# Kernel optimization log

Hardware: AMD Instinct MI355X
Metric: run time of the kernel (lower is better)

Reference implementation:

```python
import jax, jax.numpy as jnp
import numpy as np
import math

N_BINS = 2  # K: exact-enumeration branch requires K**R <= 1024


def setup_inputs() -> dict:
    key = jax.random.key(0)
    # activity in [0,1): B=131072 samples, R=10 binary components -> K**R = 1024 joint states
    activity = jax.random.uniform(key, (131072, 10), dtype=jnp.float32)
    return {"activity": activity}


def reference(activity):
    B, R = activity.shape
    K = N_BINS
    # soft assignment for n_bins == 2: [B, R, K]
    soft_assign = jnp.stack([1.0 - activity, activity], axis=-1)
    # exact joint distribution via sequential outer-product expansion: [B, K**R]
    joint_p = soft_assign[:, 0, :]
    for r in range(1, R):  # fixed small structural loop over R components
        joint_p = (joint_p[:, :, None] * soft_assign[:, r, None, :]).reshape(B, -1)
    p_a = joint_p.mean(axis=0)                      # [K**R]
    p_a_safe = jnp.clip(p_a, 1e-12)
    log_k_p = jnp.log(p_a_safe) / math.log(K)       # log base K
    joint_h = -jnp.sum(p_a * log_k_p)
    return -joint_h
```

## Files before the change

### kernel.cpp

```cpp
#include <hip/hip_runtime.h>
#include <hip/hip_bf16.h>
#include <math.h>

#define NBINS   1024
#define NPART   1024
#define NCHUNK  32
#define LSTRIDE 72

typedef __attribute__((ext_vector_type(8)))  short short8;
typedef __attribute__((ext_vector_type(16))) float f32x16;


__global__ __launch_bounds__(128, 2) void hist_kernel(const float* __restrict__ act,
                                                      float* __restrict__ gC,
                                                      int rows)
{
    __shared__ ushort Phi_u[2][32][LSTRIDE];
    __shared__ ushort Plo_u[2][32][LSTRIDE];
    __shared__ float  C_lds[NBINS];

    const int tid  = threadIdx.x;
    const int wav  = tid >> 6;
    const int lane = tid & 63;

    const int row = blockIdx.x * 128 + tid;

    float v[10];
    float valid = 1.0f;
    if (row < rows) {
        const float2* a2 = (const float2*)(act + (size_t)row * 10);
        #pragma unroll
        for (int k = 0; k < 5; ++k) {
            float2 t = a2[k];
            v[2 * k] = t.x; v[2 * k + 1] = t.y;
        }
    } else {
        valid = 0.0f;
        #pragma unroll
        for (int k = 0; k < 10; ++k) v[k] = 0.0f;
    }

    float hi[32], lo[32];
    {
        float t2[2], t4[4], t8[8], t16[16];
        t2[0] = valid * (1.0f - v[0]); t2[1] = valid * v[0];
        #pragma unroll
        for (int k = 0; k < 4; ++k)  t4[k]  = t2[k >> 1]  * ((k & 1) ? v[1] : 1.0f - v[1]);
        #pragma unroll
        for (int k = 0; k < 8; ++k)  t8[k]  = t4[k >> 1]  * ((k & 1) ? v[2] : 1.0f - v[2]);
        #pragma unroll
        for (int k = 0; k < 16; ++k) t16[k] = t8[k >> 1]  * ((k & 1) ? v[3] : 1.0f - v[3]);
        #pragma unroll
        for (int k = 0; k < 32; ++k) hi[k]  = t16[k >> 1] * ((k & 1) ? v[4] : 1.0f - v[4]);
    }
    {
        float t2[2], t4[4], t8[8], t16[16];
        t2[0] = 1.0f - v[5]; t2[1] = v[5];
        #pragma unroll
        for (int k = 0; k < 4; ++k)  t4[k]  = t2[k >> 1]  * ((k & 1) ? v[6] : 1.0f - v[6]);
        #pragma unroll
        for (int k = 0; k < 8; ++k)  t8[k]  = t4[k >> 1]  * ((k & 1) ? v[7] : 1.0f - v[7]);
        #pragma unroll
        for (int k = 0; k < 16; ++k) t16[k] = t8[k >> 1]  * ((k & 1) ? v[8] : 1.0f - v[8]);
        #pragma unroll
        for (int k = 0; k < 32; ++k) lo[k]  = t16[k >> 1] * ((k & 1) ? v[9] : 1.0f - v[9]);
    }

    #pragma unroll
    for (int m = 0; m < 32; ++m) {
        __hip_bfloat16 bh = __float2bfloat16(hi[m]);
        __hip_bfloat16 bl = __float2bfloat16(lo[m]);
        Phi_u[wav][m][lane] = *(const ushort*)&bh;
        Plo_u[wav][m][lane] = *(const ushort*)&bl;
    }

    __syncthreads();

    const int m  = lane & 31;
    const int kh = (lane >> 5) * 8;

    f32x16 acc = {};
    #pragma unroll
    for (int t = 0; t < 4; ++t) {
        const short8 a = *(const short8*)&Phi_u[wav][m][kh + 16 * t];
        const short8 b = *(const short8*)&Plo_u[wav][m][kh + 16 * t];
        acc = __builtin_amdgcn_mfma_f32_32x32x16_bf16(a, b, acc, 0, 0, 0);
    }

    if (wav == 1) {
        #pragma unroll
        for (int r = 0; r < 16; ++r)
            C_lds[r * 64 + lane] = acc[r];
    }
    __syncthreads();
    if (wav == 0) {
        #pragma unroll
        for (int r = 0; r < 16; ++r)
            C_lds[r * 64 + lane] += acc[r];
    }
    __syncthreads();

    float4* dst4 = (float4*)(gC + (size_t)blockIdx.x * NBINS);
    const float4* src4 = (const float4*)C_lds;
    dst4[tid]       = src4[tid];
    dst4[tid + 128] = src4[tid + 128];
}

__global__ __launch_bounds__(256) void reduce_kernel(const float* __restrict__ gC,
                                                     float* __restrict__ g2)
{
    const int chunk = blockIdx.x >> 2;
    const int bin   = (blockIdx.x & 3) * 256 + threadIdx.x;
    const float* p  = gC + (size_t)chunk * 32 * NBINS + bin;
    float s = 0.0f;
    #pragma unroll
    for (int k = 0; k < 32; ++k) s += p[k * NBINS];
    g2[chunk * NBINS + bin] = s;
}

__global__ __launch_bounds__(256) void finalize_kernel(const float* __restrict__ g2,
                                                       float* __restrict__ out,
                                                       float invB)
{
    __shared__ float red[4];
    const int tid = threadIdx.x;

    float4 acc = make_float4(0.f, 0.f, 0.f, 0.f);
    #pragma unroll
    for (int s = 0; s < NCHUNK; ++s) {
        const float4 t = *(const float4*)&g2[s * NBINS + tid * 4];
        acc.x += t.x; acc.y += t.y; acc.z += t.z; acc.w += t.w;
    }

    float s = 0.0f;
    const float b[4] = {acc.x, acc.y, acc.z, acc.w};
    #pragma unroll
    for (int k = 0; k < 4; ++k) {
        const float p  = b[k] * invB;
        const float ps = fmaxf(p, 1e-12f);
        s += p * log2f(ps);
    }
    #pragma unroll
    for (int off = 32; off > 0; off >>= 1) s += __shfl_down(s, off);
    if ((tid & 63) == 0) red[tid >> 6] = s;
    __syncthreads();
    if (tid == 0) out[0] = red[0] + red[1] + red[2] + red[3];
}

extern "C" void kernel_launch(void* const* d_in, const int* in_sizes, int n_in,
                              void* d_out, int out_size, void* d_ws, size_t ws_size,
                              hipStream_t stream)
{
    const float* act = (const float*)d_in[0];
    const int rows = in_sizes[0] / 10;
    float* gC = (float*)d_ws;
    float* g2 = gC + 1024 * NBINS;

    hist_kernel<<<NPART, 128, 0, stream>>>(act, gC, rows);
    reduce_kernel<<<128, 256, 0, stream>>>(gC, g2);
    finalize_kernel<<<1, 256, 0, stream>>>(g2, (float*)d_out, 1.0f / (float)rows);
}
```

Baseline: 16.46 us.

## Process two row tiles per block to halve partial histograms

Each hist block now handles 256 rows in two sequential MFMA passes that share one accumulator, and the grid shrinks from 1024 to 512 blocks. This halves the partial-histogram traffic written to workspace and read back by the reduce kernel, which now sums 16 partials per chunk instead of 32. The cost is an extra pair of barriers and LDS reuse per block, less parallelism in the histogram stage, and higher register pressure from keeping both rows' inputs live.

```diff
diff --git a/kernel.cpp b/kernel.cpp
--- a/kernel.cpp
+++ b/kernel.cpp
@@ -3,44 +3,18 @@
 #include <math.h>
 
 #define NBINS   1024
-#define NPART   1024
+#define NPART   512
 #define NCHUNK  32
+#define PPC     16
 #define LSTRIDE 72
 
 typedef __attribute__((ext_vector_type(8)))  short short8;
 typedef __attribute__((ext_vector_type(16))) float f32x16;
 
 
-__global__ __launch_bounds__(128, 2) void hist_kernel(const float* __restrict__ act,
-                                                      float* __restrict__ gC,
-                                                      int rows)
+__device__ __forceinline__ void make_trees(const float v[10], float valid,
+                                           float hi[32], float lo[32])
 {
-    __shared__ ushort Phi_u[2][32][LSTRIDE];
-    __shared__ ushort Plo_u[2][32][LSTRIDE];
-    __shared__ float  C_lds[NBINS];
-
-    const int tid  = threadIdx.x;
-    const int wav  = tid >> 6;
-    const int lane = tid & 63;
-
-    const int row = blockIdx.x * 128 + tid;
-
-    float v[10];
-    float valid = 1.0f;
-    if (row < rows) {
-        const float2* a2 = (const float2*)(act + (size_t)row * 10);
-        #pragma unroll
-        for (int k = 0; k < 5; ++k) {
-            float2 t = a2[k];
-            v[2 * k] = t.x; v[2 * k + 1] = t.y;
-        }
-    } else {
-        valid = 0.0f;
-        #pragma unroll
-        for (int k = 0; k < 10; ++k) v[k] = 0.0f;
-    }
-
-    float hi[32], lo[32];
     {
         float t2[2], t4[4], t8[8], t16[16];
         t2[0] = valid * (1.0f - v[0]); t2[1] = valid * v[0];
@@ -65,26 +39,84 @@
         #pragma unroll
         for (int k = 0; k < 32; ++k) lo[k]  = t16[k >> 1] * ((k & 1) ? v[9] : 1.0f - v[9]);
     }
+}
 
-    #pragma unroll
-    for (int m = 0; m < 32; ++m) {
-        __hip_bfloat16 bh = __float2bfloat16(hi[m]);
-        __hip_bfloat16 bl = __float2bfloat16(lo[m]);
-        Phi_u[wav][m][lane] = *(const ushort*)&bh;
-        Plo_u[wav][m][lane] = *(const ushort*)&bl;
+__global__ __launch_bounds__(128, 2) void hist_kernel(const float* __restrict__ act,
+                                                      float* __restrict__ gC,
+                                                      int rows)
+{
+    __shared__ ushort Phi_u[2][32][LSTRIDE];
+    __shared__ ushort Plo_u[2][32][LSTRIDE];
+    __shared__ float  C_lds[NBINS];
+
+    const int tid  = threadIdx.x;
+    const int wav  = tid >> 6;
+    const int lane = tid & 63;
+
+    const int r0 = blockIdx.x * 256 + tid;
+    const int r1 = r0 + 128;
+
+    float v0[10], v1[10];
+    float valid0 = 1.0f, valid1 = 1.0f;
+    if (r0 < rows) {
+        const float2* a2 = (const float2*)(act + (size_t)r0 * 10);
+        #pragma unroll
+        for (int k = 0; k < 5; ++k) { float2 t = a2[k]; v0[2*k] = t.x; v0[2*k+1] = t.y; }
+    } else {
+        valid0 = 0.0f;
+        #pragma unroll
+        for (int k = 0; k < 10; ++k) v0[k] = 0.0f;
     }
-
-    __syncthreads();
+    if (r1 < rows) {
+        const float2* a2 = (const float2*)(act + (size_t)r1 * 10);
+        #pragma unroll
+        for (int k = 0; k < 5; ++k) { float2 t = a2[k]; v1[2*k] = t.x; v1[2*k+1] = t.y; }
+    } else {
+        valid1 = 0.0f;
+        #pragma unroll
+        for (int k = 0; k < 10; ++k) v1[k] = 0.0f;
+    }
 
     const int m  = lane & 31;
     const int kh = (lane >> 5) * 8;
+    f32x16 acc = {};
 
-    f32x16 acc = {};
-    #pragma unroll
-    for (int t = 0; t < 4; ++t) {
-        const short8 a = *(const short8*)&Phi_u[wav][m][kh + 16 * t];
-        const short8 b = *(const short8*)&Plo_u[wav][m][kh + 16 * t];
-        acc = __builtin_amdgcn_mfma_f32_32x32x16_bf16(a, b, acc, 0, 0, 0);
+    {
+        float hi[32], lo[32];
+        make_trees(v0, valid0, hi, lo);
+        #pragma unroll
+        for (int q = 0; q < 32; ++q) {
+            __hip_bfloat16 bh = __float2bfloat16(hi[q]);
+            __hip_bfloat16 bl = __float2bfloat16(lo[q]);
+            Phi_u[wav][q][lane] = *(const ushort*)&bh;
+            Plo_u[wav][q][lane] = *(const ushort*)&bl;
+        }
+        __syncthreads();
+        #pragma unroll
+        for (int t = 0; t < 4; ++t) {
+            const short8 a = *(const short8*)&Phi_u[wav][m][kh + 16 * t];
+            const short8 b = *(const short8*)&Plo_u[wav][m][kh + 16 * t];
+            acc = __builtin_amdgcn_mfma_f32_32x32x16_bf16(a, b, acc, 0, 0, 0);
+        }
+        __syncthreads();
+    }
+    {
+        float hi[32], lo[32];
+        make_trees(v1, valid1, hi, lo);
+        #pragma unroll
+        for (int q = 0; q < 32; ++q) {
+            __hip_bfloat16 bh = __float2bfloat16(hi[q]);
+            __hip_bfloat16 bl = __float2bfloat16(lo[q]);
+            Phi_u[wav][q][lane] = *(const ushort*)&bh;
+            Plo_u[wav][q][lane] = *(const ushort*)&bl;
+        }
+        __syncthreads();
+        #pragma unroll
+        for (int t = 0; t < 4; ++t) {
+            const short8 a = *(const short8*)&Phi_u[wav][m][kh + 16 * t];
+            const short8 b = *(const short8*)&Plo_u[wav][m][kh + 16 * t];
+            acc = __builtin_amdgcn_mfma_f32_32x32x16_bf16(a, b, acc, 0, 0, 0);
+        }
     }
 
     if (wav == 1) {
@@ -111,10 +143,10 @@
 {
     const int chunk = blockIdx.x >> 2;
     const int bin   = (blockIdx.x & 3) * 256 + threadIdx.x;
-    const float* p  = gC + (size_t)chunk * 32 * NBINS + bin;
+    const float* p  = gC + (size_t)chunk * PPC * NBINS + bin;
     float s = 0.0f;
     #pragma unroll
-    for (int k = 0; k < 32; ++k) s += p[k * NBINS];
+    for (int k = 0; k < PPC; ++k) s += p[k * NBINS];
     g2[chunk * NBINS + bin] = s;
 }
 
@@ -154,7 +186,7 @@
     const float* act = (const float*)d_in[0];
     const int rows = in_sizes[0] / 10;
     float* gC = (float*)d_ws;
-    float* g2 = gC + 1024 * NBINS;
+    float* g2 = gC + (size_t)NPART * NBINS;
 
     hist_kernel<<<NPART, 128, 0, stream>>>(act, gC, rows);
     reduce_kernel<<<128, 256, 0, stream>>>(gC, g2);
```

Result: no change. 16.27 us (-1.1%).
